# Kernel optimization log

Measured on AMD Instinct MI355X. Metric: run time of the kernel, lower is better.

## Reference

```python
import jax, jax.numpy as jnp
import numpy as np
from jax import lax

B, T, D_IN, H = 1024, 256, 6, 128
EPS = 1e-5


def layer_norm(x, g, b):
    mu = jnp.mean(x, axis=-1, keepdims=True)
    var = jnp.mean((x - mu) ** 2, axis=-1, keepdims=True)
    return (x - mu) * lax.rsqrt(var + EPS) * g + b


def lstm_dir(x, Wih, Whh, bih, bhh, reverse):
    # x: [B,T,Din]; Wih: [4H,Din]; Whh: [4H,H]. PyTorch gate order: i,f,g,o.
    xp = jnp.einsum('btd,gd->btg', x, Wih) + bih + bhh  # [B,T,4H]
    h0 = jnp.zeros((x.shape[0], Whh.shape[1]), x.dtype)
    c0 = jnp.zeros_like(h0)

    def step(carry, xt):
        h, c = carry
        gates = xt + h @ Whh.T
        i, f, g, o = jnp.split(gates, 4, axis=-1)
        c = jax.nn.sigmoid(f) * c + jax.nn.sigmoid(i) * jnp.tanh(g)
        h = jax.nn.sigmoid(o) * jnp.tanh(c)
        return (h, c), h

    _, hs = lax.scan(step, (h0, c0), jnp.swapaxes(xp, 0, 1), reverse=reverse)
    return jnp.swapaxes(hs, 0, 1)  # [B,T,H], aligned to input time order


def bilstm_layer(x, Wih, Whh, bih, bhh):
    # direction-stacked params: Wih [2,4H,Din], etc.
    fwd = lstm_dir(x, Wih[0], Whh[0], bih[0], bhh[0], reverse=False)
    bwd = lstm_dir(x, Wih[1], Whh[1], bih[1], bhh[1], reverse=True)
    return jnp.concatenate([fwd, bwd], axis=-1)  # [B,T,2H]


def setup_inputs() -> dict:
    key = jax.random.key(0)
    ks = iter(jax.random.split(key, 32))
    u = lambda shape, s: jax.random.uniform(next(ks), shape, jnp.float32, -s, s)
    s_h = 1.0 / np.sqrt(H)
    inp = {
        'x': jax.random.normal(next(ks), (B, T, D_IN), jnp.float32),
        'ln_g': jnp.ones((D_IN,), jnp.float32),
        'ln_b': jnp.zeros((D_IN,), jnp.float32),
        'Wih0': u((2, 4 * H, D_IN), s_h), 'Whh0': u((2, 4 * H, H), s_h),
        'bih0': u((2, 4 * H), s_h), 'bhh0': u((2, 4 * H), s_h),
        'Wih1': u((2, 4 * H, 2 * H), s_h), 'Whh1': u((2, 4 * H, H), s_h),
        'bih1': u((2, 4 * H), s_h), 'bhh1': u((2, 4 * H), s_h),
        'Wa1': u((H, 2 * H), 1.0 / np.sqrt(2 * H)), 'ba1': jnp.zeros((H,), jnp.float32),
        'Wa2': u((1, H), s_h), 'ba2': jnp.zeros((1,), jnp.float32),
        'Wf1': u((H, 2 * H), 1.0 / np.sqrt(2 * H)), 'bf1': jnp.zeros((H,), jnp.float32),
        'ln2_g': jnp.ones((H,), jnp.float32), 'ln2_b': jnp.zeros((H,), jnp.float32),
        'Wf2': u((5, H), s_h),
        'bf2': jnp.array([0.0, 0.0, -0.7, -0.7, 0.0], jnp.float32),
    }
    return inp


def reference(x, ln_g, ln_b, Wih0, Whh0, bih0, bhh0, Wih1, Whh1, bih1, bhh1,
              Wa1, ba1, Wa2, ba2, Wf1, bf1, ln2_g, ln2_b, Wf2, bf2):
    x = layer_norm(x, ln_g, ln_b)
    h = bilstm_layer(x, Wih0, Whh0, bih0, bhh0)       # [B,T,2H]
    h = bilstm_layer(h, Wih1, Whh1, bih1, bhh1)       # [B,T,2H] (eval: no dropout)
    scores = jnp.tanh(h @ Wa1.T + ba1) @ Wa2.T + ba2  # [B,T,1]
    attn = jax.nn.softmax(scores, axis=1)
    context = jnp.sum(h * attn, axis=1)               # [B,2H]
    z = jax.nn.relu(layer_norm(context @ Wf1.T + bf1, ln2_g, ln2_b))
    return z @ Wf2.T + bf2                            # [B,5]
```

## Files before the change

kernel.cpp:

```cpp
#include <hip/hip_runtime.h>
#include <stdint.h>

#define TT 256
#define NS 8
#define CH 8
#define L2E 1.4426950408889634f
#define L2E2 2.8853900817779268f

typedef __attribute__((ext_vector_type(4))) float f32x4;
typedef __attribute__((ext_vector_type(8))) short s16x8;
typedef __attribute__((ext_vector_type(2))) unsigned int u32x2;

#define DEV static __device__ __forceinline__

__device__ uint16_t g_W1f[2*32*8*64*8];

DEV short f2bf(float f){
  union{float f; uint32_t u;} v; v.f = f;
  uint32_t r = v.u + 0x7fffu + ((v.u>>16)&1u);
  return (short)(r>>16);
}
DEV float bf2f(uint32_t u16){
  union{uint32_t u; float f;} v; v.u = u16<<16; return v.f;
}
DEV uint32_t pk2(float a, float b){
  return (uint32_t)(uint16_t)f2bf(a) | ((uint32_t)(uint16_t)f2bf(b)<<16);
}
DEV float rcpf(float x){ return __builtin_amdgcn_rcpf(x); }
DEV float exp2fast(float x){ return __builtin_amdgcn_exp2f(x); }
DEV float sigm2(float x){ return rcpf(1.f + exp2fast(-x)); }
DEV float tanh2(float x){ return 1.f - 2.f*rcpf(exp2fast(x) + 1.f); }
DEV float tanhr(float x){ return 1.f - 2.f*rcpf(exp2fast(L2E2*x) + 1.f); }
DEV f32x4 MFMA(s16x8 a, s16x8 b, f32x4 c){
  return __builtin_amdgcn_mfma_f32_16x16x32_bf16(a, b, c, 0, 0, 0);
}
DEV s16x8 cvt8(const float* p){
  f32x4 a = *(const f32x4*)p;
  f32x4 b = *(const f32x4*)(p+4);
  s16x8 o;
  o[0]=f2bf(a[0]); o[1]=f2bf(a[1]); o[2]=f2bf(a[2]); o[3]=f2bf(a[3]);
  o[4]=f2bf(b[0]); o[5]=f2bf(b[1]); o[6]=f2bf(b[2]); o[7]=f2bf(b[3]);
  return o;
}
DEV s16x8 cvt8s(const float* p, float s){
  f32x4 a = *(const f32x4*)p;
  f32x4 b = *(const f32x4*)(p+4);
  s16x8 o;
  o[0]=f2bf(a[0]*s); o[1]=f2bf(a[1]*s); o[2]=f2bf(a[2]*s); o[3]=f2bf(a[3]*s);
  o[4]=f2bf(b[0]*s); o[5]=f2bf(b[1]*s); o[6]=f2bf(b[2]*s); o[7]=f2bf(b[3]*s);
  return o;
}
DEV void bar_lds(){
  asm volatile("s_waitcnt lgkmcnt(0)" ::: "memory");
  __builtin_amdgcn_s_barrier();
}

DEV void flush_step(const short* hb, uint16_t* __restrict__ hdst, int tp,
                    int dir, int BR, int bg, int tid){
  if (tid < 128){
    int row = tid >> 4, part = tid & 15;
    int tg = dir ? (TT-1-tp) : tp;
    s16x8 v = *(const s16x8*)((const char*)hb + row*256 + (((part ^ row)&15)<<4));
    *(s16x8*)(hdst + ((size_t)tg*BR + bg*NS + row)*256 + dir*128 + part*8) = v;
  }
}

__global__ __launch_bounds__(256) void prep_wih1(const float* __restrict__ Wih1)
{
  int tid = blockIdx.x*256 + threadIdx.x;
  int l = tid & 63, kt = (tid>>6)&7, ntg = (tid>>9)&31, dir = (tid>>14)&1;
  int lm = l&15, lk = l>>4;
  int n = ntg*16 + lm;
  float sc = ((ntg>>3) == 2) ? L2E2 : L2E;
  s16x8 o = cvt8s(Wih1 + ((size_t)(dir*512 + n))*256 + kt*32 + lk*8, sc);
  *(s16x8*)(&g_W1f[(size_t)tid*8]) = o;
}

__global__ __launch_bounds__(512,2) void lstm0_kernel(
    const float* __restrict__ x, const float* __restrict__ lng,
    const float* __restrict__ lnb,
    const float* __restrict__ Wih0, const float* __restrict__ Whh0,
    const float* __restrict__ bih0, const float* __restrict__ bhh0,
    uint16_t* __restrict__ h0, int nb, int BR, int b_off)
{
  const int dir = blockIdx.x / nb, bg = blockIdx.x % nb;
  const int tid = threadIdx.x, w = tid>>6, l = tid&63;
  const int lm = l&15, lk = l>>4;
  const int gb = b_off + bg*NS;

  __shared__ short hbuf[2][2048];
  __shared__ short xnbf[TT*NS*8];
  __shared__ short bxs[8*4*64*8];

  for (int i=tid; i<4096; i+=512) ((short*)hbuf)[i] = 0;

  #pragma unroll
  for (int it=0; it<4; ++it){
    int pr = it*512 + tid;
    int r = pr >> 8, t = pr & 255;
    const float* px = x + ((size_t)(gb+r)*TT + t)*6;
    float v[6]; float mu=0.f, var=0.f;
    #pragma unroll
    for (int d=0; d<6; ++d){ v[d]=px[d]; mu+=v[d]; }
    mu *= (1.f/6.f);
    #pragma unroll
    for (int d=0; d<6; ++d){ float dd=v[d]-mu; var+=dd*dd; }
    float rs = rsqrtf(var*(1.f/6.f) + 1e-5f);
    s16x8 vv;
    #pragma unroll
    for (int d=0; d<6; ++d) vv[d] = f2bf((v[d]-mu)*rs*lng[d] + lnb[d]);
    vv[6]=0; vv[7]=0;
    *(s16x8*)&xnbf[(t*NS + r)*8] = vv;
  }

  const int c = w*16 + lm;
  s16x8 bw[4][4];
  float biasc[4];
  #pragma unroll
  for (int G=0; G<4; ++G){
    const float sc = (G==2) ? L2E2 : L2E;
    const int n = G*128 + c;
    biasc[G] = (bih0[dir*512+n] + bhh0[dir*512+n])*sc;
    #pragma unroll
    for (int kt=0; kt<4; ++kt)
      bw[G][kt] = cvt8s(Whh0 + ((size_t)(dir*512+n))*128 + kt*32 + lk*8, sc);
    s16x8 tx;
    #pragma unroll
    for (int j=0; j<8; ++j){
      int k = lk*8 + j;
      tx[j] = (k<6) ? f2bf(Wih0[(size_t)(dir*512+n)*6 + k]*sc) : (short)0;
    }
    *(s16x8*)&bxs[((w*4+G)*64 + l)*8] = tx;
  }

  const int r0 = ((l>>4)&1)*4 + ((l<32)?0:2);
  float cst[2] = {0.f, 0.f};
  __syncthreads();

  for (int t=0; t<TT; ++t){
    const int tt = dir ? (TT-1-t) : t;
    const int rd = t & 1;
    s16x8 ah[4];
    #pragma unroll
    for (int kt=0; kt<4; ++kt){
      int off = rd*4096 + lm*256 + ((kt*64 + lk*16) ^ (lm<<4));
      ah[kt] = *(const s16x8*)((const char*)hbuf + off);
    }
    s16x8 ax = {0,0,0,0,0,0,0,0};
    if (l < 8) ax = *(const s16x8*)&xnbf[(tt*NS + l)*8];

    f32x4 acc[4];
    #pragma unroll
    for (int G=0; G<4; ++G){
      f32x4 a = {0.f,0.f,0.f,0.f};
      #pragma unroll
      for (int kt=0; kt<4; ++kt) a = MFMA(ah[kt], bw[G][kt], a);
      s16x8 bx = *(const s16x8*)&bxs[((w*4+G)*64 + l)*8];
      a = MFMA(ax, bx, a);
      acc[G] = a;
    }

    float g0[4], g1[4];
    #pragma unroll
    for (int G=0; G<4; ++G){
      float o2 = __shfl(acc[G][2], l & 31);
      float o3 = __shfl(acc[G][3], l & 31);
      g0[G] = ((l<32) ? acc[G][0] : o2) + biasc[G];
      g1[G] = ((l<32) ? acc[G][1] : o3) + biasc[G];
    }
    float hv[2];
    {
      float cc = sigm2(g0[1])*cst[0] + sigm2(g0[0])*tanh2(g0[2]);
      cst[0] = cc; hv[0] = sigm2(g0[3])*tanhr(cc);
      cc = sigm2(g1[1])*cst[1] + sigm2(g1[0])*tanh2(g1[2]);
      cst[1] = cc; hv[1] = sigm2(g1[3])*tanhr(cc);
    }

    #pragma unroll
    for (int q=0; q<2; ++q){
      int r = r0 + q;
      *(short*)((char*)hbuf + (rd^1)*4096 + r*256 + ((c*2) ^ (r<<4))) = f2bf(hv[q]);
    }
    if (t > 0)
      flush_step(hbuf[rd], h0, t-1, dir, BR, bg, tid);
    bar_lds();
  }
  flush_step(hbuf[0], h0, TT-1, dir, BR, bg, tid);
}

__global__ __launch_bounds__(512,2) void lstm1_kernel(
    const uint16_t* __restrict__ h0,
    const float* __restrict__ Whh1, const float* __restrict__ bih1,
    const float* __restrict__ bhh1, uint16_t* __restrict__ h1,
    int nb, int BR)
{
  const int dir = blockIdx.x / nb, bg = blockIdx.x % nb;
  const int tid = threadIdx.x, w = tid>>6, l = tid&63;
  const int lm = l&15, lk = l>>4;

  __shared__ short hbuf[2][2048];
  __shared__ short abuf[2][16384];
  __shared__ u32x2 xpbuf[8192];

  for (int i=tid; i<4096; i+=512) ((short*)hbuf)[i] = 0;

  const int c = w*16 + lm;
  s16x8 bw[4][4];
  float biasv[4];
  #pragma unroll
  for (int G=0; G<4; ++G){
    const float sc = (G==2) ? L2E2 : L2E;
    const int n = G*128 + c;
    biasv[G] = (bih1[dir*512+n] + bhh1[dir*512+n])*sc;
    #pragma unroll
    for (int kt=0; kt<4; ++kt)
      bw[G][kt] = cvt8s(Whh1 + ((size_t)(dir*512+n))*128 + kt*32 + lk*8, sc);
  }

  const int r0 = ((l>>4)&1)*4 + ((l<32)?0:2);
  float cst[2] = {0.f,0.f};
  s16x8 vst[4];

  #pragma unroll
  for (int it=0; it<4; ++it){
    int sid = it*512 + tid, row = sid>>5, sl = sid&31, s = row>>3, b = row&7;
    int tg = dir ? (TT-1-s) : s;
    vst[it] = *(const s16x8*)(h0 + ((size_t)tg*BR + bg*NS + b)*256 + sl*8);
  }
  #pragma unroll
  for (int it=0; it<4; ++it){
    int sid = it*512 + tid, row = sid>>5, sl = sid&31;
    *(s16x8*)((char*)abuf + row*512 + ((sl ^ (row&15))<<4)) = vst[it];
  }
  __syncthreads();

  for (int ch=0; ch<TT/CH; ++ch){
    const int cur = ch & 1;
    const char* ab = (const char*)abuf + cur*32768;

    if (ch < TT/CH-1){
      #pragma unroll
      for (int it=0; it<4; ++it){
        int sid = it*512 + tid, row = sid>>5, sl = sid&31, s = row>>3, b = row&7;
        int ts = (ch+1)*CH + s;
        int tg = dir ? (TT-1-ts) : ts;
        vst[it] = *(const s16x8*)(h0 + ((size_t)tg*BR + bg*NS + b)*256 + sl*8);
      }
    }

    #pragma unroll
    for (int G=0; G<4; ++G){
      f32x4 acc[4];
      #pragma unroll
      for (int mt=0; mt<4; ++mt) acc[mt] = (f32x4){biasv[G],biasv[G],biasv[G],biasv[G]};
      #pragma unroll
      for (int kt=0; kt<8; ++kt){
        s16x8 bfr = *(const s16x8*)(&g_W1f[(((size_t)(dir*32 + G*8 + w)*8 + kt)*64 + l)*8]);
        #pragma unroll
        for (int mt=0; mt<4; ++mt){
          int row = mt*16 + lm;
          s16x8 afr = *(const s16x8*)(ab + row*512 + (((kt*4+lk) ^ (row&15))<<4));
          acc[mt] = MFMA(afr, bfr, acc[mt]);
        }
      }
      #pragma unroll
      for (int mt=0; mt<4; ++mt){
        u32x2 pw;
        pw[0] = pk2(acc[mt][0], acc[mt][1]);
        pw[1] = pk2(acc[mt][2], acc[mt][3]);
        xpbuf[((w*4+G)*4+mt)*64 + l] = pw;
      }
    }

    if (ch < TT/CH-1){
      char* ab2 = (char*)abuf + (cur^1)*32768;
      #pragma unroll
      for (int it=0; it<4; ++it){
        int sid = it*512 + tid, row = sid>>5, sl = sid&31;
        *(s16x8*)(ab2 + row*512 + ((sl ^ (row&15))<<4)) = vst[it];
      }
    }
    bar_lds();

    #pragma unroll
    for (int s=0; s<CH; ++s){
      const int gs = ch*CH + s;
      const int rd = gs & 1;
      const int lane2 = ((((s&1)<<1) + lk)<<4) + lm;

      f32x4 acc4[4];
      #pragma unroll
      for (int G=0; G<4; ++G){
        u32x2 pw = xpbuf[((w*4+G)*4 + (s>>1))*64 + lane2];
        acc4[G] = (f32x4){bf2f(pw[0]&0xffffu), bf2f(pw[0]>>16),
                          bf2f(pw[1]&0xffffu), bf2f(pw[1]>>16)};
      }

      s16x8 ah[4];
      #pragma unroll
      for (int kt=0; kt<4; ++kt){
        int off = rd*4096 + lm*256 + ((kt*64 + lk*16) ^ (lm<<4));
        ah[kt] = *(const s16x8*)((const char*)hbuf + off);
      }
      #pragma unroll
      for (int G=0; G<4; ++G){
        #pragma unroll
        for (int kt=0; kt<4; ++kt)
          acc4[G] = MFMA(ah[kt], bw[G][kt], acc4[G]);
      }

      float g0[4], g1[4];
      #pragma unroll
      for (int G=0; G<4; ++G){
        float o2 = __shfl(acc4[G][2], l & 31);
        float o3 = __shfl(acc4[G][3], l & 31);
        g0[G] = (l<32) ? acc4[G][0] : o2;
        g1[G] = (l<32) ? acc4[G][1] : o3;
      }
      float hv[2];
      float cc = sigm2(g0[1])*cst[0] + sigm2(g0[0])*tanh2(g0[2]);
      cst[0] = cc; hv[0] = sigm2(g0[3])*tanhr(cc);
      cc = sigm2(g1[1])*cst[1] + sigm2(g1[0])*tanh2(g1[2]);
      cst[1] = cc; hv[1] = sigm2(g1[3])*tanhr(cc);

      #pragma unroll
      for (int q=0; q<2; ++q){
        int r = r0 + q;
        *(short*)((char*)hbuf + (rd^1)*4096 + r*256 + ((c*2) ^ (r<<4))) = f2bf(hv[q]);
      }
      if (gs > 0)
        flush_step(hbuf[rd], h1, gs-1, dir, BR, bg, tid);
      bar_lds();
    }
  }
  flush_step(hbuf[0], h1, TT-1, dir, BR, bg, tid);
}

__global__ __launch_bounds__(256,2) void att_kernel(
    const uint16_t* __restrict__ h1,
    const float* __restrict__ Wa1, const float* __restrict__ ba1,
    const float* __restrict__ Wa2, const float* __restrict__ ba2,
    const float* __restrict__ Wf1, const float* __restrict__ bf1,
    const float* __restrict__ lg, const float* __restrict__ lb,
    const float* __restrict__ Wf2, const float* __restrict__ bf2v,
    float* __restrict__ out, int BR, int b_off)
{
  const int b = blockIdx.x;
  const int tid = threadIdx.x, w = tid>>6, l = tid&63;
  const int lm = l&15, lk = l>>4;

  __shared__ short abuf[64*256];
  __shared__ float sbuf[TT];
  __shared__ float scred[4][64];
  __shared__ float red[8];
  __shared__ float cbuf[256];
  __shared__ float zb[128];

  s16x8 bwa[2][8]; float b1v[2], wa2v[2];
  #pragma unroll
  for (int nt=0; nt<2; ++nt){
    int n = w*32 + nt*16 + lm;
    b1v[nt] = ba1[n]; wa2v[nt] = Wa2[n];
    #pragma unroll
    for (int kt=0; kt<8; ++kt)
      bwa[nt][kt] = cvt8(Wa1 + (size_t)n*256 + kt*32 + lk*8);
  }

  for (int tb=0; tb<4; ++tb){
    const int t0 = tb*64;
    __syncthreads();
    #pragma unroll
    for (int it=0; it<8; ++it){
      int sid = it*256 + tid, row = sid>>5, sl = sid&31;
      s16x8 v = *(const s16x8*)(h1 + ((size_t)(t0+row)*BR + b)*256 + sl*8);
      *(s16x8*)((char*)abuf + row*512 + ((sl ^ (row&15))<<4)) = v;
    }
    __syncthreads();

    #pragma unroll
    for (int mt=0; mt<4; ++mt){
      f32x4 a0 = {b1v[0],b1v[0],b1v[0],b1v[0]};
      f32x4 a1 = {b1v[1],b1v[1],b1v[1],b1v[1]};
      #pragma unroll
      for (int kt=0; kt<8; ++kt){
        int row = mt*16 + lm;
        s16x8 af = *(const s16x8*)((const char*)abuf + row*512 + (((kt*4+lk) ^ (row&15))<<4));
        a0 = MFMA(af, bwa[0][kt], a0);
        a1 = MFMA(af, bwa[1][kt], a1);
      }
      #pragma unroll
      for (int j=0; j<4; ++j){
        float pj = tanhr(a0[j])*wa2v[0] + tanhr(a1[j])*wa2v[1];
        #pragma unroll
        for (int m2=1; m2<16; m2<<=1) pj += __shfl_xor(pj, m2);
        if (lm == 0) scred[w][mt*16 + lk*4 + j] = pj;
      }
    }
    __syncthreads();
    if (tid < 64)
      sbuf[t0 + tid] = scred[0][tid]+scred[1][tid]+scred[2][tid]+scred[3][tid] + ba2[0];
  }
  __syncthreads();

  float scv = sbuf[tid];
  float m = scv;
  #pragma unroll
  for (int d=1; d<64; d<<=1) m = fmaxf(m, __shfl_xor(m, d));
  if (l == 0) red[w] = m;
  __syncthreads();
  m = fmaxf(fmaxf(red[0],red[1]), fmaxf(red[2],red[3]));
  float e = exp2fast(L2E*(scv - m));
  float ssum = e;
  #pragma unroll
  for (int d=1; d<64; d<<=1) ssum += __shfl_xor(ssum, d);
  if (l == 0) red[4+w] = ssum;
  __syncthreads();
  ssum = red[4]+red[5]+red[6]+red[7];
  sbuf[tid] = e * rcpf(ssum);
  __syncthreads();

  float acc = 0.f;
  const uint16_t* hp = h1 + (size_t)b*256 + tid;
  #pragma unroll 8
  for (int t2=0; t2<TT; ++t2) acc += sbuf[t2] * bf2f(hp[(size_t)t2*BR*256]);
  cbuf[tid] = acc;
  __syncthreads();

  float y = 0.f;
  if (tid < 128){
    y = bf1[tid];
    const float* wr = Wf1 + (size_t)tid*256;
    #pragma unroll 8
    for (int k=0; k<256; ++k) y += cbuf[k]*wr[k];
  }
  float s2 = y;
  #pragma unroll
  for (int d=1; d<64; d<<=1) s2 += __shfl_xor(s2, d);
  if (l == 0) red[w] = s2;
  __syncthreads();
  float mu = (red[0]+red[1]+red[2]+red[3])*(1.f/128.f);
  float dv = y - mu;
  float q = (tid < 128) ? dv*dv : 0.f;
  #pragma unroll
  for (int d=1; d<64; d<<=1) q += __shfl_xor(q, d);
  if (l == 0) red[4+w] = q;
  __syncthreads();
  float var = (red[4]+red[5]+red[6]+red[7])*(1.f/128.f);
  if (tid < 128){
    float z = dv*rsqrtf(var + 1e-5f)*lg[tid] + lb[tid];
    zb[tid] = fmaxf(z, 0.f);
  }
  __syncthreads();
  if (tid < 5){
    float o = bf2v[tid];
    const float* wp = Wf2 + (size_t)tid*128;
    for (int k=0; k<128; ++k) o += zb[k]*wp[k];
    out[(size_t)(b_off + b)*5 + tid] = o;
  }
}

extern "C" void kernel_launch(void* const* d_in, const int* in_sizes, int n_in,
                              void* d_out, int out_size, void* d_ws, size_t ws_size,
                              hipStream_t stream)
{
  const float* x    = (const float*)d_in[0];
  const float* ln_g = (const float*)d_in[1];
  const float* ln_b = (const float*)d_in[2];
  const float* Wih0 = (const float*)d_in[3];
  const float* Whh0 = (const float*)d_in[4];
  const float* bih0 = (const float*)d_in[5];
  const float* bhh0 = (const float*)d_in[6];
  const float* Wih1 = (const float*)d_in[7];
  const float* Whh1 = (const float*)d_in[8];
  const float* bih1 = (const float*)d_in[9];
  const float* bhh1 = (const float*)d_in[10];
  const float* Wa1  = (const float*)d_in[11];
  const float* ba1  = (const float*)d_in[12];
  const float* Wa2  = (const float*)d_in[13];
  const float* ba2  = (const float*)d_in[14];
  const float* Wf1  = (const float*)d_in[15];
  const float* bf1  = (const float*)d_in[16];
  const float* ln2g = (const float*)d_in[17];
  const float* ln2b = (const float*)d_in[18];
  const float* Wf2  = (const float*)d_in[19];
  const float* bf2  = (const float*)d_in[20];
  float* out = (float*)d_out;

  char* wsb = (char*)d_ws;
  const size_t HBf = (size_t)TT*1024*256*2;

  prep_wih1<<<128, 256, 0, stream>>>(Wih1);

  if (ws_size >= 2*HBf){
    uint16_t* h0 = (uint16_t*)wsb;
    uint16_t* h1 = (uint16_t*)(wsb + HBf);

    lstm0_kernel<<<256, 512, 0, stream>>>(x, ln_g, ln_b, Wih0, Whh0, bih0, bhh0,
                                          h0, 128, 1024, 0);
    lstm1_kernel<<<256, 512, 0, stream>>>(h0, Whh1, bih1, bhh1, h1, 128, 1024);
    att_kernel  <<<1024, 256, 0, stream>>>(h1, Wa1, ba1, Wa2, ba2, Wf1, bf1,
                                           ln2g, ln2b, Wf2, bf2, out, 1024, 0);
  } else {
    int BR = 512;
    while (BR > 64){
      size_t HB = (size_t)TT*BR*256*2;
      if (2*HB <= ws_size) break;
      BR >>= 1;
    }
    const size_t HB = (size_t)TT*BR*256*2;
    uint16_t* h0 = (uint16_t*)wsb;
    uint16_t* h1 = (uint16_t*)(wsb + HB);
    const int nb = BR/NS;

    for (int b_off = 0; b_off < 1024; b_off += BR){
      lstm0_kernel<<<2*nb, 512, 0, stream>>>(x, ln_g, ln_b, Wih0, Whh0, bih0, bhh0,
                                             h0, nb, BR, b_off);
      lstm1_kernel<<<2*nb, 512, 0, stream>>>(h0, Whh1, bih1, bhh1, h1, nb, BR);
      att_kernel  <<<BR, 256, 0, stream>>>(h1, Wa1, ba1, Wa2, ba2, Wf1, bf1,
                                           ln2g, ln2b, Wf2, bf2, out, BR, b_off);
    }
  }
}
```

Baseline: 724.1 us.

## Add 4-row-per-block LSTM kernels to spread recurrence over more workgroups

```diff
diff --git a/kernel.cpp b/kernel.cpp
--- a/kernel.cpp
+++ b/kernel.cpp
@@ -62,6 +62,15 @@
     int tg = dir ? (TT-1-tp) : tp;
     s16x8 v = *(const s16x8*)((const char*)hb + row*256 + (((part ^ row)&15)<<4));
     *(s16x8*)(hdst + ((size_t)tg*BR + bg*NS + row)*256 + dir*128 + part*8) = v;
+  }
+}
+DEV void flush_step4(const short* hb, uint16_t* __restrict__ hdst, int tp,
+                     int dir, int BR, int bg, int tid){
+  if (tid < 64){
+    int row = tid >> 4, part = tid & 15;
+    int tg = dir ? (TT-1-tp) : tp;
+    s16x8 v = *(const s16x8*)((const char*)hb + row*256 + (((part ^ row)&15)<<4));
+    *(s16x8*)(hdst + ((size_t)tg*BR + bg*4 + row)*256 + dir*128 + part*8) = v;
   }
 }
 
@@ -334,6 +343,289 @@
     }
   }
   flush_step(hbuf[0], h1, TT-1, dir, BR, bg, tid);
+}
+
+__global__ __launch_bounds__(256,1) void lstm0_wide(
+    const float* __restrict__ x, const float* __restrict__ lng,
+    const float* __restrict__ lnb,
+    const float* __restrict__ Wih0, const float* __restrict__ Whh0,
+    const float* __restrict__ bih0, const float* __restrict__ bhh0,
+    uint16_t* __restrict__ h0, int nb, int BR, int b_off)
+{
+  const int dir = blockIdx.x / nb, bg = blockIdx.x % nb;
+  const int tid = threadIdx.x, w = tid>>6, l = tid&63;
+  const int lm = l&15, lk = l>>4;
+  const int gb = b_off + bg*4;
+
+  __shared__ short hbuf[2][2048];
+  __shared__ short xnbf[TT*4*8];
+  __shared__ short bxs[8*4*64*8];
+
+  for (int i=tid; i<4096; i+=256) ((short*)hbuf)[i] = 0;
+
+  #pragma unroll
+  for (int it=0; it<4; ++it){
+    int pr = it*256 + tid;
+    int r = pr >> 8, t = pr & 255;
+    const float* px = x + ((size_t)(gb+r)*TT + t)*6;
+    float v[6]; float mu=0.f, var=0.f;
+    #pragma unroll
+    for (int d=0; d<6; ++d){ v[d]=px[d]; mu+=v[d]; }
+    mu *= (1.f/6.f);
+    #pragma unroll
+    for (int d=0; d<6; ++d){ float dd=v[d]-mu; var+=dd*dd; }
+    float rs = rsqrtf(var*(1.f/6.f) + 1e-5f);
+    s16x8 vv;
+    #pragma unroll
+    for (int d=0; d<6; ++d) vv[d] = f2bf((v[d]-mu)*rs*lng[d] + lnb[d]);
+    vv[6]=0; vv[7]=0;
+    *(s16x8*)&xnbf[(t*4 + r)*8] = vv;
+  }
+
+  int cc2[2];
+  s16x8 bw[2][4][4];
+  float biasc[2][4];
+  #pragma unroll
+  for (int cg=0; cg<2; ++cg){
+    const int cgid = w + cg*4;
+    const int c = cgid*16 + lm;
+    cc2[cg] = c;
+    #pragma unroll
+    for (int G=0; G<4; ++G){
+      const float sc = (G==2) ? L2E2 : L2E;
+      const int n = G*128 + c;
+      biasc[cg][G] = (bih0[dir*512+n] + bhh0[dir*512+n])*sc;
+      #pragma unroll
+      for (int kt=0; kt<4; ++kt)
+        bw[cg][G][kt] = cvt8s(Whh0 + ((size_t)(dir*512+n))*128 + kt*32 + lk*8, sc);
+      s16x8 tx;
+      #pragma unroll
+      for (int j=0; j<8; ++j){
+        int k = lk*8 + j;
+        tx[j] = (k<6) ? f2bf(Wih0[(size_t)(dir*512+n)*6 + k]*sc) : (short)0;
+      }
+      *(s16x8*)&bxs[((cgid*4+G)*64 + l)*8] = tx;
+    }
+  }
+
+  const int r0 = ((l>>4)&1)*4 + ((l<32)?0:2);
+  float cst[2][2] = {{0.f,0.f},{0.f,0.f}};
+  __syncthreads();
+
+  for (int t=0; t<TT; ++t){
+    const int tt = dir ? (TT-1-t) : t;
+    const int rd = t & 1;
+    s16x8 ah[4];
+    #pragma unroll
+    for (int kt=0; kt<4; ++kt){
+      int off = rd*4096 + lm*256 + ((kt*64 + lk*16) ^ (lm<<4));
+      ah[kt] = *(const s16x8*)((const char*)hbuf + off);
+    }
+    s16x8 ax = {0,0,0,0,0,0,0,0};
+    if (l < 4) ax = *(const s16x8*)&xnbf[(tt*4 + l)*8];
+
+    #pragma unroll
+    for (int cg=0; cg<2; ++cg){
+      const int cgid = w + cg*4;
+      f32x4 acc[4];
+      #pragma unroll
+      for (int G=0; G<4; ++G){
+        f32x4 a = {0.f,0.f,0.f,0.f};
+        #pragma unroll
+        for (int kt=0; kt<4; ++kt) a = MFMA(ah[kt], bw[cg][G][kt], a);
+        s16x8 bx = *(const s16x8*)&bxs[((cgid*4+G)*64 + l)*8];
+        a = MFMA(ax, bx, a);
+        acc[G] = a;
+      }
+      float g0[4], g1[4];
+      #pragma unroll
+      for (int G=0; G<4; ++G){
+        float o2 = __shfl(acc[G][2], l & 31);
+        float o3 = __shfl(acc[G][3], l & 31);
+        g0[G] = ((l<32) ? acc[G][0] : o2) + biasc[cg][G];
+        g1[G] = ((l<32) ? acc[G][1] : o3) + biasc[cg][G];
+      }
+      float c0 = sigm2(g0[1])*cst[cg][0] + sigm2(g0[0])*tanh2(g0[2]);
+      cst[cg][0] = c0;
+      float hv0 = sigm2(g0[3])*tanhr(c0);
+      float c1 = sigm2(g1[1])*cst[cg][1] + sigm2(g1[0])*tanh2(g1[2]);
+      cst[cg][1] = c1;
+      float hv1 = sigm2(g1[3])*tanhr(c1);
+
+      if (r0 < 4){
+        const int c = cc2[cg];
+        *(short*)((char*)hbuf + (rd^1)*4096 + r0*256 + ((c*2) ^ (r0<<4))) = f2bf(hv0);
+        int r = r0+1;
+        *(short*)((char*)hbuf + (rd^1)*4096 + r*256 + ((c*2) ^ (r<<4))) = f2bf(hv1);
+      }
+    }
+    if (t > 0)
+      flush_step4(hbuf[rd], h0, t-1, dir, BR, bg, tid);
+    bar_lds();
+  }
+  flush_step4(hbuf[0], h0, TT-1, dir, BR, bg, tid);
+}
+
+__global__ __launch_bounds__(256,1) void lstm1_wide(
+    const uint16_t* __restrict__ h0,
+    const float* __restrict__ Whh1, const float* __restrict__ bih1,
+    const float* __restrict__ bhh1, uint16_t* __restrict__ h1,
+    int nb, int BR)
+{
+  const int dir = blockIdx.x / nb, bg = blockIdx.x % nb;
+  const int tid = threadIdx.x, w = tid>>6, l = tid&63;
+  const int lm = l&15, lk = l>>4;
+
+  __shared__ short hbuf[2][2048];
+  __shared__ short abuf[2][8192];
+  __shared__ u32x2 xpbuf[4096];
+
+  for (int i=tid; i<4096; i+=256) ((short*)hbuf)[i] = 0;
+
+  int cc2[2];
+  s16x8 bw[2][4][4];
+  float biasv[2][4];
+  #pragma unroll
+  for (int cg=0; cg<2; ++cg){
+    const int c = (w + cg*4)*16 + lm;
+    cc2[cg] = c;
+    #pragma unroll
+    for (int G=0; G<4; ++G){
+      const float sc = (G==2) ? L2E2 : L2E;
+      const int n = G*128 + c;
+      biasv[cg][G] = (bih1[dir*512+n] + bhh1[dir*512+n])*sc;
+      #pragma unroll
+      for (int kt=0; kt<4; ++kt)
+        bw[cg][G][kt] = cvt8s(Whh1 + ((size_t)(dir*512+n))*128 + kt*32 + lk*8, sc);
+    }
+  }
+
+  const int r0 = ((l>>4)&1)*4 + ((l<32)?0:2);
+  float cst[2][2] = {{0.f,0.f},{0.f,0.f}};
+  s16x8 vst[4];
+
+  #pragma unroll
+  for (int it=0; it<4; ++it){
+    int sid = it*256 + tid, row = sid>>5, sl = sid&31, s = row>>2, b = row&3;
+    int tg = dir ? (TT-1-s) : s;
+    vst[it] = *(const s16x8*)(h0 + ((size_t)tg*BR + bg*4 + b)*256 + sl*8);
+  }
+  #pragma unroll
+  for (int it=0; it<4; ++it){
+    int sid = it*256 + tid, row = sid>>5, sl = sid&31;
+    *(s16x8*)((char*)abuf + row*512 + ((sl ^ (row&15))<<4)) = vst[it];
+  }
+  __syncthreads();
+
+  for (int ch=0; ch<TT/CH; ++ch){
+    const int cur = ch & 1;
+    const char* ab = (const char*)abuf + cur*16384;
+
+    if (ch < TT/CH-1){
+      #pragma unroll
+      for (int it=0; it<4; ++it){
+        int sid = it*256 + tid, row = sid>>5, sl = sid&31, s = row>>2, b = row&3;
+        int ts = (ch+1)*CH + s;
+        int tg = dir ? (TT-1-ts) : ts;
+        vst[it] = *(const s16x8*)(h0 + ((size_t)tg*BR + bg*4 + b)*256 + sl*8);
+      }
+    }
+
+    #pragma unroll
+    for (int cg=0; cg<2; ++cg){
+      const int cgid = w + cg*4;
+      #pragma unroll
+      for (int G=0; G<4; ++G){
+        f32x4 acc[2];
+        #pragma unroll
+        for (int mt=0; mt<2; ++mt)
+          acc[mt] = (f32x4){biasv[cg][G],biasv[cg][G],biasv[cg][G],biasv[cg][G]};
+        #pragma unroll
+        for (int kt=0; kt<8; ++kt){
+          s16x8 bfr = *(const s16x8*)(&g_W1f[(((size_t)(dir*32 + G*8 + cgid)*8 + kt)*64 + l)*8]);
+          #pragma unroll
+          for (int mt=0; mt<2; ++mt){
+            int row = mt*16 + lm;
+            s16x8 afr = *(const s16x8*)(ab + row*512 + (((kt*4+lk) ^ (row&15))<<4));
+            acc[mt] = MFMA(afr, bfr, acc[mt]);
+          }
+        }
+        #pragma unroll
+        for (int mt=0; mt<2; ++mt){
+          u32x2 pw;
+          pw[0] = pk2(acc[mt][0], acc[mt][1]);
+          pw[1] = pk2(acc[mt][2], acc[mt][3]);
+          xpbuf[((cgid*4+G)*2+mt)*64 + l] = pw;
+        }
+      }
+    }
+
+    if (ch < TT/CH-1){
+      char* ab2 = (char*)abuf + (cur^1)*16384;
+      #pragma unroll
+      for (int it=0; it<4; ++it){
+        int sid = it*256 + tid, row = sid>>5, sl = sid&31;
+        *(s16x8*)(ab2 + row*512 + ((sl ^ (row&15))<<4)) = vst[it];
+      }
+    }
+    bar_lds();
+
+    #pragma unroll
+    for (int s=0; s<CH; ++s){
+      const int gs = ch*CH + s;
+      const int rd = gs & 1;
+      const int lane2 = ((s&3)<<4) + lm;
+      const int mt = s>>2;
+
+      s16x8 ah[4];
+      #pragma unroll
+      for (int kt=0; kt<4; ++kt){
+        int off = rd*4096 + lm*256 + ((kt*64 + lk*16) ^ (lm<<4));
+        ah[kt] = *(const s16x8*)((const char*)hbuf + off);
+      }
+
+      #pragma unroll
+      for (int cg=0; cg<2; ++cg){
+        const int cgid = w + cg*4;
+        f32x4 acc4[4];
+        #pragma unroll
+        for (int G=0; G<4; ++G){
+          u32x2 pw = xpbuf[((cgid*4+G)*2 + mt)*64 + lane2];
+          acc4[G] = (f32x4){bf2f(pw[0]&0xffffu), bf2f(pw[0]>>16),
+                            bf2f(pw[1]&0xffffu), bf2f(pw[1]>>16)};
+          #pragma unroll
+          for (int kt=0; kt<4; ++kt)
+            acc4[G] = MFMA(ah[kt], bw[cg][G][kt], acc4[G]);
+        }
+
+        float g0[4], g1[4];
+        #pragma unroll
+        for (int G=0; G<4; ++G){
+          float o2 = __shfl(acc4[G][2], l & 31);
+          float o3 = __shfl(acc4[G][3], l & 31);
+          g0[G] = (l<32) ? acc4[G][0] : o2;
+          g1[G] = (l<32) ? acc4[G][1] : o3;
+        }
+        float c0 = sigm2(g0[1])*cst[cg][0] + sigm2(g0[0])*tanh2(g0[2]);
+        cst[cg][0] = c0;
+        float hv0 = sigm2(g0[3])*tanhr(c0);
+        float c1 = sigm2(g1[1])*cst[cg][1] + sigm2(g1[0])*tanh2(g1[2]);
+        cst[cg][1] = c1;
+        float hv1 = sigm2(g1[3])*tanhr(c1);
+
+        if (r0 < 4){
+          const int c = cc2[cg];
+          *(short*)((char*)hbuf + (rd^1)*4096 + r0*256 + ((c*2) ^ (r0<<4))) = f2bf(hv0);
+          int r = r0+1;
+          *(short*)((char*)hbuf + (rd^1)*4096 + r*256 + ((c*2) ^ (r<<4))) = f2bf(hv1);
+        }
+      }
+      if (gs > 0)
+        flush_step4(hbuf[rd], h1, gs-1, dir, BR, bg, tid);
+      bar_lds();
+    }
+  }
+  flush_step4(hbuf[0], h1, TT-1, dir, BR, bg, tid);
 }
 
 __global__ __launch_bounds__(256,2) void att_kernel(
@@ -486,6 +778,15 @@
   const float* bf2  = (const float*)d_in[20];
   float* out = (float*)d_out;
 
+  bool wide0 = false, wide1 = false;
+  {
+    hipFuncAttributes fa;
+    if (hipFuncGetAttributes(&fa, (const void*)lstm0_wide) == hipSuccess &&
+        fa.localSizeBytes == 0 && fa.numRegs <= 256) wide0 = true;
+    if (hipFuncGetAttributes(&fa, (const void*)lstm1_wide) == hipSuccess &&
+        fa.localSizeBytes == 0 && fa.numRegs <= 256) wide1 = true;
+  }
+
   char* wsb = (char*)d_ws;
   const size_t HBf = (size_t)TT*1024*256*2;
 
@@ -495,9 +796,16 @@
     uint16_t* h0 = (uint16_t*)wsb;
     uint16_t* h1 = (uint16_t*)(wsb + HBf);
 
-    lstm0_kernel<<<256, 512, 0, stream>>>(x, ln_g, ln_b, Wih0, Whh0, bih0, bhh0,
-                                          h0, 128, 1024, 0);
-    lstm1_kernel<<<256, 512, 0, stream>>>(h0, Whh1, bih1, bhh1, h1, 128, 1024);
+    if (wide0)
+      lstm0_wide<<<512, 256, 0, stream>>>(x, ln_g, ln_b, Wih0, Whh0, bih0, bhh0,
+                                          h0, 256, 1024, 0);
+    else
+      lstm0_kernel<<<256, 512, 0, stream>>>(x, ln_g, ln_b, Wih0, Whh0, bih0, bhh0,
+                                            h0, 128, 1024, 0);
+    if (wide1)
+      lstm1_wide<<<512, 256, 0, stream>>>(h0, Whh1, bih1, bhh1, h1, 256, 1024);
+    else
+      lstm1_kernel<<<256, 512, 0, stream>>>(h0, Whh1, bih1, bhh1, h1, 128, 1024);
     att_kernel  <<<1024, 256, 0, stream>>>(h1, Wa1, ba1, Wa2, ba2, Wf1, bf1,
                                            ln2g, ln2b, Wf2, bf2, out, 1024, 0);
   } else {
@@ -510,14 +818,20 @@
     const size_t HB = (size_t)TT*BR*256*2;
     uint16_t* h0 = (uint16_t*)wsb;
     uint16_t* h1 = (uint16_t*)(wsb + HB);
-    const int nb = BR/NS;
 
     for (int b_off = 0; b_off < 1024; b_off += BR){
-      lstm0_kernel<<<2*nb, 512, 0, stream>>>(x, ln_g, ln_b, Wih0, Whh0, bih0, bhh0,
-                                             h0, nb, BR, b_off);
-      lstm1_kernel<<<2*nb, 512, 0, stream>>>(h0, Whh1, bih1, bhh1, h1, nb, BR);
-      att_kernel  <<<BR, 256, 0, stream>>>(h1, Wa1, ba1, Wa2, ba2, Wf1, bf1,
-                                           ln2g, ln2b, Wf2, bf2, out, BR, b_off);
-    }
-  }
-}
+      if (wide0)
+        lstm0_wide<<<2*(BR/4), 256, 0, stream>>>(x, ln_g, ln_b, Wih0, Whh0, bih0, bhh0,
+                                                 h0, BR/4, BR, b_off);
+      else
+        lstm0_kernel<<<2*(BR/8), 512, 0, stream>>>(x, ln_g, ln_b, Wih0, Whh0, bih0, bhh0,
+                                                   h0, BR/8, BR, b_off);
+      if (wide1)
+        lstm1_wide<<<2*(BR/4), 256, 0, stream>>>(h0, Whh1, bih1, bhh1, h1, BR/4, BR);
+      else
+        lstm1_kernel<<<2*(BR/8), 512, 0, stream>>>(h0, Whh1, bih1, bhh1, h1, BR/8, BR);
+      att_kernel<<<BR, 256, 0, stream>>>(h1, Wa1, ba1, Wa2, ba2, Wf1, bf1,
+                                         ln2g, ln2b, Wf2, bf2, out, BR, b_off);
+    }
+  }
+}
```

Measured after the change: 723.5 us. Within noise of the previous version (-0.1%).
